# Kernel tuning notes

Measured on AMD Instinct MI355X. Metric: run time of the kernel, lower is better.

Reference implementation:

```python
import jax, jax.numpy as jnp
import numpy as np

H = 1024
NUM_HEADS = 16
HEAD_DIM = H // NUM_HEADS
EPS = 1e-6
GEN_E, GEN_IE = 8, 4096 // 8     # general experts, per-expert intermediate
MOD_E, MOD_IE = 4, 4096 // 4     # per-modality experts, per-expert intermediate


def layernorm(x, g, b):
    m = jnp.mean(x, axis=-1, keepdims=True)
    v = jnp.mean((x - m) ** 2, axis=-1, keepdims=True)
    return (x - m) * jax.lax.rsqrt(v + EPS) * g + b


def attention(x, qkv_w, qkv_b, proj_w, proj_b):
    B, N, _ = x.shape
    qkv = (x @ qkv_w + qkv_b).reshape(B, N, 3, NUM_HEADS, HEAD_DIM)
    qkv = jnp.transpose(qkv, (2, 0, 3, 1, 4))  # [3,B,h,N,d]
    q, k, v = qkv[0], qkv[1], qkv[2]
    scale = HEAD_DIM ** -0.5
    attn = jax.nn.softmax(jnp.einsum('bhnd,bhmd->bhnm', q, k) * scale, axis=-1)
    out = jnp.einsum('bhnm,bhmd->bhnd', attn, v)
    out = jnp.transpose(out, (0, 2, 1, 3)).reshape(B, N, H)
    return out @ proj_w + proj_b


def routed_mlp(x, position_ids, gate_up, down, ie):
    # expert_id = position % num_experts; compute all experts then select per token
    # (avoids materializing per-token [T,H,2I] gathered weights).
    E = gate_up.shape[0]
    eids = position_ids % E  # [B,N]
    gu = jnp.einsum('bnh,ehi->bnei', x, gate_up)              # [B,N,E,2*ie]
    gu = jnp.take_along_axis(gu, eids[..., None, None], axis=2)[:, :, 0]
    gate, up = gu[..., :ie], gu[..., ie:]
    inter = jax.nn.silu(gate) * up                             # [B,N,ie]
    dn = jnp.einsum('bni,eih->bneh', inter, down)              # [B,N,E,H]
    return jnp.take_along_axis(dn, eids[..., None, None], axis=2)[:, :, 0]


def setup_inputs() -> dict:
    key = jax.random.key(0)
    ks = jax.random.split(key, 16)
    B, N = 2, 2048
    inp = {
        'x': jax.random.normal(ks[0], (B, N, H), jnp.float32),
        'qkv_w': jax.random.normal(ks[1], (H, 3 * H), jnp.float32) * 0.02,
        'qkv_b': jnp.zeros((3 * H,), jnp.float32),
        'proj_w': jax.random.normal(ks[2], (H, H), jnp.float32) * 0.02,
        'proj_b': jnp.zeros((H,), jnp.float32),
        'ln1_g': jnp.ones((H,), jnp.float32), 'ln1_b': jnp.zeros((H,), jnp.float32),
        'ln2_g': jnp.ones((H,), jnp.float32), 'ln2_b': jnp.zeros((H,), jnp.float32),
        'ln3_g': jnp.ones((H,), jnp.float32), 'ln3_b': jnp.zeros((H,), jnp.float32),
        'gen_gu': jax.random.normal(ks[3], (GEN_E, H, 2 * GEN_IE), jnp.float32) * 0.02,
        'gen_dn': jax.random.normal(ks[4], (GEN_E, GEN_IE, H), jnp.float32) * 0.02,
        'text_gu': jax.random.normal(ks[5], (MOD_E, H, 2 * MOD_IE), jnp.float32) * 0.02,
        'text_dn': jax.random.normal(ks[6], (MOD_E, MOD_IE, H), jnp.float32) * 0.02,
        'img_gu': jax.random.normal(ks[7], (MOD_E, H, 2 * MOD_IE), jnp.float32) * 0.02,
        'img_dn': jax.random.normal(ks[8], (MOD_E, MOD_IE, H), jnp.float32) * 0.02,
        'aud_gu': jax.random.normal(ks[9], (MOD_E, H, 2 * MOD_IE), jnp.float32) * 0.02,
        'aud_dn': jax.random.normal(ks[10], (MOD_E, MOD_IE, H), jnp.float32) * 0.02,
        'vid_gu': jax.random.normal(ks[11], (MOD_E, H, 2 * MOD_IE), jnp.float32) * 0.02,
        'vid_dn': jax.random.normal(ks[12], (MOD_E, MOD_IE, H), jnp.float32) * 0.02,
        'modality_ids': jax.random.randint(ks[13], (B, N), 0, 4, jnp.int32),
        'position_ids': jnp.arange(B * N, dtype=jnp.int32).reshape(B, N),
    }
    return inp


def reference(x, qkv_w, qkv_b, proj_w, proj_b,
              ln1_g, ln1_b, ln2_g, ln2_b, ln3_g, ln3_b,
              gen_gu, gen_dn, text_gu, text_dn, img_gu, img_dn,
              aud_gu, aud_dn, vid_gu, vid_dn,
              modality_ids, position_ids):
    x = x + attention(layernorm(x, ln1_g, ln1_b), qkv_w, qkv_b, proj_w, proj_b)
    x = x + routed_mlp(layernorm(x, ln2_g, ln2_b), position_ids, gen_gu, gen_dn, GEN_IE)
    normed = layernorm(x, ln3_g, ln3_b)
    tm = (modality_ids == 0)[..., None].astype(x.dtype)
    im = (modality_ids == 1)[..., None].astype(x.dtype)
    am = (modality_ids == 2)[..., None].astype(x.dtype)
    vm = (modality_ids == 3)[..., None].astype(x.dtype)
    x = x + (routed_mlp(normed, position_ids, text_gu, text_dn, MOD_IE) * tm
             + routed_mlp(normed, position_ids, img_gu, img_dn, MOD_IE) * im
             + routed_mlp(normed, position_ids, aud_gu, aud_dn, MOD_IE) * am
             + routed_mlp(normed, position_ids, vid_gu, vid_dn, MOD_IE) * vm)
    return x
```

## Files before the change

kernel.cpp:

```cpp
#include <hip/hip_runtime.h>

#define T_TOKENS 4096
#define HDIM 1024

typedef __attribute__((ext_vector_type(8))) short bf16x8;
typedef __attribute__((ext_vector_type(4))) float f32x4;

#define EXP2F(x) __builtin_amdgcn_exp2f(x)

static __device__ inline unsigned short f2bf(float f) {
  unsigned u = __float_as_uint(f);
  unsigned r = (u + 0x7FFFu + ((u >> 16) & 1u)) >> 16;
  return (unsigned short)r;
}
static __device__ __forceinline__ unsigned cvtpk(float lo, float hi) {
  unsigned r;
  asm("v_cvt_pk_bf16_f32 %0, %1, %2" : "=v"(r) : "v"(lo), "v"(hi));
  return r;
}
static __device__ __forceinline__ void gl16(const void* g, void* l) {
  __builtin_amdgcn_global_load_lds((const __attribute__((address_space(1))) void*)g,
                                   (__attribute__((address_space(3))) void*)l, 16, 0, 0);
}

__launch_bounds__(256)
__global__ void ln_kernel(const float* __restrict__ in, const float* __restrict__ g,
                          const float* __restrict__ b, unsigned short* __restrict__ out) {
  const int row = blockIdx.x;
  const int tid = threadIdx.x;
  const long base = (long)row * HDIM;
  float4 v = *(const float4*)(in + base + tid * 4);
  __shared__ float red[256];
  red[tid] = v.x + v.y + v.z + v.w;
  __syncthreads();
  for (int st = 128; st > 0; st >>= 1) {
    if (tid < st) red[tid] += red[tid + st];
    __syncthreads();
  }
  const float mean = red[0] * (1.f / HDIM);
  __syncthreads();
  const float dx = v.x - mean, dy = v.y - mean, dz = v.z - mean, dw = v.w - mean;
  red[tid] = dx * dx + dy * dy + dz * dz + dw * dw;
  __syncthreads();
  for (int st = 128; st > 0; st >>= 1) {
    if (tid < st) red[tid] += red[tid + st];
    __syncthreads();
  }
  const float rstd = rsqrtf(red[0] * (1.f / HDIM) + 1e-6f);
  const int c = tid * 4;
  const float4 g4 = *(const float4*)(g + c);
  const float4 b4 = *(const float4*)(b + c);
  uint2 o;
  o.x = cvtpk(dx * rstd * g4.x + b4.x, dy * rstd * g4.y + b4.y);
  o.y = cvtpk(dz * rstd * g4.z + b4.z, dw * rstd * g4.w + b4.w);
  *(uint2*)(out + base + c) = o;
}

__launch_bounds__(256)
__global__ void build_groups(const int* __restrict__ pids, const int* __restrict__ mids,
                             int* __restrict__ gen_cnt, int* __restrict__ gen_list,
                             int* __restrict__ mod_cnt, int* __restrict__ mod_list) {
  const int t = blockIdx.x * 256 + threadIdx.x;
  if (t >= T_TOKENS) return;
  const int p = pids[t];
  const int ge = p & 7;
  int s = atomicAdd(&gen_cnt[ge], 1);
  if (s < 512) gen_list[ge * 512 + s] = t;
  const int g = mids[t] * 4 + (p & 3);
  s = atomicAdd(&mod_cnt[g], 1);
  if (s < 1024) mod_list[g * 1024 + s] = t;
}

__launch_bounds__(256)
__global__ void convert_w(const float* __restrict__ W, unsigned short* __restrict__ Wt,
                          int K, int N) {
  const long zo = (long)blockIdx.z * K * N;
  const float* Wp = W + zo;
  unsigned short* Wo = Wt + zo;
  const int n0 = blockIdx.x * 64, k0 = blockIdx.y * 64;
  __shared__ float T[64][65];
  const int tid = threadIdx.x;
#pragma unroll
  for (int i = 0; i < 4; ++i) {
    const int item = tid + i * 256;
    const int kk = item >> 4, c4 = (item & 15) * 4;
    const float4 v = *(const float4*)(Wp + (long)(k0 + kk) * N + n0 + c4);
    T[c4 + 0][kk] = v.x; T[c4 + 1][kk] = v.y; T[c4 + 2][kk] = v.z; T[c4 + 3][kk] = v.w;
  }
  __syncthreads();
#pragma unroll
  for (int i = 0; i < 4; ++i) {
    const int item = tid + i * 256;
    const int nn = item >> 4, k4 = (item & 15) * 4;
    uint2 p;
    p.x = cvtpk(T[nn][k4 + 0], T[nn][k4 + 1]);
    p.y = cvtpk(T[nn][k4 + 2], T[nn][k4 + 3]);
    *(uint2*)(Wo + (long)(n0 + nn) * K + k0 + k4) = p;
  }
}

enum { MODE_DENSE = 0, MODE_GEN = 1, MODE_MOD = 2 };
enum { OM_F32R = 0, OM_BF16 = 1, OM_QKV = 2 };

template <int MODE, int OMODE, bool WBF16, bool BIAS>
__launch_bounds__(256)
__global__ void mgemm(const unsigned short* __restrict__ A,
                      const void* __restrict__ w0, const float* __restrict__ w1,
                      const float* __restrict__ w2, const float* __restrict__ w3,
                      long wstep, const float* __restrict__ bias,
                      const float* __restrict__ resid, void* __restrict__ Cout,
                      unsigned short* __restrict__ qb, unsigned short* __restrict__ kb,
                      unsigned short* __restrict__ vtb,
                      int K, int N,
                      const int* __restrict__ cnts, const int* __restrict__ rowlist,
                      int cap) {
  const int z = blockIdx.z;
  const int n0 = blockIdx.x * 128;
  const int m0 = blockIdx.y * 128;

  int Meff = 1 << 30;
  const int* list = nullptr;
  if constexpr (MODE != MODE_DENSE) {
    Meff = cnts[z];
    if (m0 >= Meff) return;
    list = rowlist + z * cap;
  }

  constexpr int BUFSZ = 128 * 64 * 2;
  __shared__ char As[2 * BUFSZ];
  __shared__ char Bs[2 * BUFSZ];

  const int tid = threadIdx.x;
  const int w = tid >> 6;
  const int lane = tid & 63;
  const int wm = w >> 1, wn = w & 1;
  const int srow = lane >> 3, sc = lane & 7;

  const unsigned short* asrc[4];
#pragma unroll
  for (int i = 0; i < 4; ++i) {
    const int r = w * 32 + i * 8 + srow;
    long tok;
    if constexpr (MODE == MODE_DENSE) {
      tok = m0 + r;
    } else {
      int gm = m0 + r;
      if (gm >= Meff) gm = Meff - 1;
      tok = (long)list[gm];
    }
    asrc[i] = A + tok * (long)K + (sc ^ (r & 7)) * 8;
  }

  const unsigned short* bsrc[4];
  const float* bptr[4];
  int boff[4];
  if constexpr (WBF16) {
    const unsigned short* W = (const unsigned short*)w0;
    if constexpr (MODE != MODE_DENSE) W += (long)z * wstep;
#pragma unroll
    for (int i = 0; i < 4; ++i) {
      const int r = w * 32 + i * 8 + srow;
      bsrc[i] = W + (long)(n0 + r) * K + (sc ^ (r & 7)) * 8;
    }
  } else {
    const float* W;
    if constexpr (MODE == MODE_MOD) {
      const int mm = z >> 2;
      const float* basep = (mm == 0) ? (const float*)w0 : (mm == 1) ? w1 : (mm == 2) ? w2 : w3;
      W = basep + (long)(z & 3) * wstep;
    } else {
      W = (const float*)w0 + (MODE != MODE_DENSE ? (long)z * wstep : 0);
    }
#pragma unroll
    for (int j = 0; j < 4; ++j) {
      const int item = tid + j * 256;
      const int kc = item >> 7;
      const int nl = item & 127;
      bptr[j] = W + (long)(kc * 8) * N + n0 + nl;
      boff[j] = (nl * 128 + kc * 16) ^ ((nl & 7) << 4);
    }
  }

  f32x4 acc[4][4] = {};
  float kv[4][8];

  auto stageA = [&](int s, int kt) {
#pragma unroll
    for (int i = 0; i < 4; ++i) gl16(asrc[i] + kt, As + s * BUFSZ + w * 4096 + i * 1024);
  };
  auto stageB16 = [&](int s, int kt) {
#pragma unroll
    for (int i = 0; i < 4; ++i) gl16(bsrc[i] + kt, Bs + s * BUFSZ + w * 4096 + i * 1024);
  };
  auto loadB = [&](int kt) {
#pragma unroll
    for (int j = 0; j < 4; ++j) {
      const float* bp = bptr[j] + (long)kt * N;
#pragma unroll
      for (int u = 0; u < 8; ++u) kv[j][u] = bp[(long)u * N];
    }
  };
  auto writeB = [&](int s) {
#pragma unroll
    for (int j = 0; j < 4; ++j) {
      uint4 p;
      p.x = cvtpk(kv[j][0], kv[j][1]);
      p.y = cvtpk(kv[j][2], kv[j][3]);
      p.z = cvtpk(kv[j][4], kv[j][5]);
      p.w = cvtpk(kv[j][6], kv[j][7]);
      *(uint4*)(Bs + s * BUFSZ + boff[j]) = p;
    }
  };
  auto compute = [&](int s) {
#pragma unroll
    for (int kk = 0; kk < 2; ++kk) {
      const int kb2 = kk * 64 + (lane >> 4) * 16;
      bf16x8 af[4], bfr[4];
#pragma unroll
      for (int f = 0; f < 4; ++f) {
        const int ar = wm * 64 + f * 16 + (lane & 15);
        af[f] = *(bf16x8*)(As + s * BUFSZ + ((ar * 128 + kb2) ^ ((ar & 7) << 4)));
        const int br = wn * 64 + f * 16 + (lane & 15);
        bfr[f] = *(bf16x8*)(Bs + s * BUFSZ + ((br * 128 + kb2) ^ ((br & 7) << 4)));
      }
#pragma unroll
      for (int mf = 0; mf < 4; ++mf)
#pragma unroll
        for (int nf = 0; nf < 4; ++nf)
          acc[mf][nf] =
              __builtin_amdgcn_mfma_f32_16x16x32_bf16(af[mf], bfr[nf], acc[mf][nf], 0, 0, 0);
    }
  };

  const int nk = K >> 6;
  stageA(0, 0);
  if constexpr (WBF16) {
    stageB16(0, 0);
  } else {
    loadB(0);
    writeB(0);
  }
  __syncthreads();

  int sel = 0;
  for (int t = 0; t < nk; ++t) {
    const bool more = (t + 1) < nk;
    const int ktn = (t + 1) * 64;
    if (more) {
      stageA(sel ^ 1, ktn);
      if constexpr (WBF16) stageB16(sel ^ 1, ktn);
      else loadB(ktn);
    }
    compute(sel);
    if constexpr (!WBF16) {
      if (more) writeB(sel ^ 1);
    }
    __syncthreads();
    sel ^= 1;
  }

  const int lr4 = (lane >> 4) * 4;
  const int lc = lane & 15;
#pragma unroll
  for (int mf = 0; mf < 4; ++mf) {
#pragma unroll
    for (int r = 0; r < 4; ++r) {
      const int gm = m0 + wm * 64 + mf * 16 + lr4 + r;
      long orow;
      if constexpr (MODE == MODE_DENSE) {
        orow = gm;
      } else {
        if (gm >= Meff) continue;
        orow = (long)list[gm];
      }
#pragma unroll
      for (int nf = 0; nf < 4; ++nf) {
        const int gc = n0 + wn * 64 + nf * 16 + lc;
        float val = acc[mf][nf][r];
        if constexpr (BIAS) val += bias[gc];
        if constexpr (OMODE == OM_F32R) {
          val += resid[orow * (long)N + gc];
          ((float*)Cout)[orow * (long)N + gc] = val;
        } else if constexpr (OMODE == OM_BF16) {
          ((unsigned short*)Cout)[orow * (long)N + gc] = f2bf(val);
        } else {
          const int bb = (int)(orow >> 11), tl = (int)orow & 2047;
          const int seg = gc >> 10, hc = gc & 1023, h = hc >> 6, d = hc & 63;
          if (seg == 0)
            qb[(((long)(bb * 16 + h) * 2048) + tl) * 64 + d] = f2bf(val * 0.18033688011112042f);
          else if (seg == 1)
            kb[(((long)(bb * 16 + h) * 2048) + tl) * 64 + d] = f2bf(val);
          else
            vtb[((long)(bb * 16 + h) * 64 + d) * 2048 + tl] = f2bf(val);
        }
      }
    }
  }
}

__launch_bounds__(256)
__global__ void attn_kernel(const unsigned short* __restrict__ Qb,
                            const unsigned short* __restrict__ Kb,
                            const unsigned short* __restrict__ Vtb,
                            unsigned short* __restrict__ out) {
  const int qt = blockIdx.x;
  const int bh = blockIdx.y;
  const int b = bh >> 4, h = bh & 15;
  const int tid = threadIdx.x;
  const int w = tid >> 6;
  const int lane = tid & 63;
  const int g = lane >> 4;
  const int q = lane & 15;

  __shared__ char Ksb[128 * 128];
  __shared__ char Vsb[64 * 256];
  __shared__ char Psb[4 * 16 * 256];
  char* Pwb = Psb + w * 4096;

  const unsigned short* Qh = Qb + ((long)(b * 16 + h) * 2048 + qt * 64) * 64;
  const unsigned short* Kh = Kb + (long)(b * 16 + h) * 2048 * 64;
  const unsigned short* Vh = Vtb + (long)(b * 16 + h) * 64 * 2048;

  bf16x8 qf[2];
#pragma unroll
  for (int kst = 0; kst < 2; ++kst)
    qf[kst] = *(const bf16x8*)(Qh + (w * 16 + q) * 64 + kst * 32 + g * 8);

  const unsigned short* ksrc[4];
  const unsigned short* vsrc[4];
  char* kld = Ksb + w * 4096;
  char* vld = Vsb + w * 4096;
#pragma unroll
  for (int i = 0; i < 4; ++i) {
    const int r = w * 32 + i * 8 + (lane >> 3);
    ksrc[i] = Kh + (long)r * 64 + ((lane & 7) ^ (r & 7)) * 8;
    const int d = w * 16 + i * 4 + (lane >> 4);
    vsrc[i] = Vh + (long)d * 2048 + ((lane & 15) ^ (d & 7)) * 8;
  }

  float m_run = -1e30f, l_run = 0.f;
  f32x4 acc[4] = {};
  const int qsw = (q & 7) << 4;

  for (int kt = 0; kt < 16; ++kt) {
    __syncthreads();
#pragma unroll
    for (int i = 0; i < 4; ++i) gl16(ksrc[i] + (long)kt * 128 * 64, kld + i * 1024);
#pragma unroll
    for (int i = 0; i < 4; ++i) gl16(vsrc[i] + kt * 128, vld + i * 1024);
    __syncthreads();

    f32x4 sf[8];
#pragma unroll
    for (int f = 0; f < 8; ++f) {
      const int krow = f * 16 + q;
      const int sw = (krow & 7) << 4;
      const bf16x8 k0 = *(bf16x8*)(Ksb + krow * 128 + ((g * 16) ^ sw));
      const bf16x8 k1 = *(bf16x8*)(Ksb + krow * 128 + ((64 + g * 16) ^ sw));
      f32x4 t = {};
      t = __builtin_amdgcn_mfma_f32_16x16x32_bf16(k0, qf[0], t, 0, 0, 0);
      sf[f] = __builtin_amdgcn_mfma_f32_16x16x32_bf16(k1, qf[1], t, 0, 0, 0);
    }

    float mx = sf[0][0];
#pragma unroll
    for (int f = 0; f < 8; ++f) {
      mx = fmaxf(mx, fmaxf(fmaxf(sf[f][0], sf[f][1]), fmaxf(sf[f][2], sf[f][3])));
    }
    mx = fmaxf(mx, __shfl_xor(mx, 16));
    mx = fmaxf(mx, __shfl_xor(mx, 32));
    const float mn = fmaxf(m_run, mx);
    const float alpha = EXP2F(m_run - mn);
    m_run = mn;

    float ls = 0.f;
#pragma unroll
    for (int f = 0; f < 8; ++f) {
#pragma unroll
      for (int r = 0; r < 4; ++r) {
        sf[f][r] = EXP2F(sf[f][r] - mn);
      }
      ls += (sf[f][0] + sf[f][1]) + (sf[f][2] + sf[f][3]);
    }
    ls += __shfl_xor(ls, 16);
    ls += __shfl_xor(ls, 32);
    l_run = l_run * alpha + ls;

#pragma unroll
    for (int f = 0; f < 8; ++f) {
      const unsigned p0 = cvtpk(sf[f][0], sf[f][1]);
      const unsigned p1 = cvtpk(sf[f][2], sf[f][3]);
      const int base = f * 32 + g * 8;
      *(unsigned*)(Pwb + q * 256 + ((base) ^ qsw)) = p0;
      *(unsigned*)(Pwb + q * 256 + ((base + 4) ^ qsw)) = p1;
    }

#pragma unroll
    for (int r = 0; r < 4; ++r) {
      const float aO = __shfl(alpha, g * 4 + r, 64);
      acc[0][r] *= aO; acc[1][r] *= aO; acc[2][r] *= aO; acc[3][r] *= aO;
    }

#pragma unroll
    for (int kst = 0; kst < 4; ++kst) {
      const bf16x8 pa = *(bf16x8*)(Pwb + q * 256 + ((kst * 64 + g * 16) ^ qsw));
#pragma unroll
      for (int df = 0; df < 4; ++df) {
        const int vrow = df * 16 + q;
        const int vsw = (vrow & 7) << 4;
        const bf16x8 vf = *(bf16x8*)(Vsb + vrow * 256 + ((kst * 64 + g * 16) ^ vsw));
        acc[df] = __builtin_amdgcn_mfma_f32_16x16x32_bf16(pa, vf, acc[df], 0, 0, 0);
      }
    }
  }

  float linv[4];
#pragma unroll
  for (int r = 0; r < 4; ++r) linv[r] = 1.f / __shfl(l_run, g * 4 + r, 64);
  unsigned short* op = out + (long)(b * 2048 + qt * 64 + w * 16) * 1024 + h * 64;
#pragma unroll
  for (int df = 0; df < 4; ++df)
#pragma unroll
    for (int r = 0; r < 4; ++r) {
      const int row = g * 4 + r;
      op[(long)row * 1024 + df * 16 + q] = f2bf(acc[df][r] * linv[r]);
    }
}

__launch_bounds__(256)
__global__ void silu_bf(const unsigned short* __restrict__ gu, unsigned short* __restrict__ inter,
                        int IE2, int IE, int shift) {
  const int total = T_TOKENS << shift;
  for (int idx = blockIdx.x * 256 + threadIdx.x; idx < total; idx += gridDim.x * 256) {
    const int t = idx >> shift;
    const int r8 = (idx & ((1 << shift) - 1)) * 8;
    const unsigned short* gp = gu + (long)t * IE2 + r8;
    const uint4 gg = *(const uint4*)gp;
    const uint4 uu = *(const uint4*)(gp + IE);
    const unsigned gw[4] = {gg.x, gg.y, gg.z, gg.w};
    const unsigned uw[4] = {uu.x, uu.y, uu.z, uu.w};
    uint4 o;
    unsigned ow[4];
#pragma unroll
    for (int qq = 0; qq < 4; ++qq) {
      const float g0 = __uint_as_float(gw[qq] << 16);
      const float g1 = __uint_as_float(gw[qq] & 0xffff0000u);
      const float u0 = __uint_as_float(uw[qq] << 16);
      const float u1 = __uint_as_float(uw[qq] & 0xffff0000u);
      const float r0 = g0 / (1.f + __expf(-g0)) * u0;
      const float r1 = g1 / (1.f + __expf(-g1)) * u1;
      ow[qq] = cvtpk(r0, r1);
    }
    o.x = ow[0]; o.y = ow[1]; o.z = ow[2]; o.w = ow[3];
    *(uint4*)(inter + (long)t * IE + r8) = o;
  }
}

extern "C" void kernel_launch(void* const* d_in, const int* in_sizes, int n_in,
                              void* d_out, int out_size, void* d_ws, size_t ws_size,
                              hipStream_t stream) {
  const float* x       = (const float*)d_in[0];
  const float* qkv_w   = (const float*)d_in[1];
  const float* qkv_b   = (const float*)d_in[2];
  const float* proj_w  = (const float*)d_in[3];
  const float* proj_b  = (const float*)d_in[4];
  const float* ln1_g   = (const float*)d_in[5];
  const float* ln1_b   = (const float*)d_in[6];
  const float* ln2_g   = (const float*)d_in[7];
  const float* ln2_b   = (const float*)d_in[8];
  const float* ln3_g   = (const float*)d_in[9];
  const float* ln3_b   = (const float*)d_in[10];
  const float* gen_gu  = (const float*)d_in[11];
  const float* gen_dn  = (const float*)d_in[12];
  const float* text_gu = (const float*)d_in[13];
  const float* text_dn = (const float*)d_in[14];
  const float* img_gu  = (const float*)d_in[15];
  const float* img_dn  = (const float*)d_in[16];
  const float* aud_gu  = (const float*)d_in[17];
  const float* aud_dn  = (const float*)d_in[18];
  const float* vid_gu  = (const float*)d_in[19];
  const float* vid_dn  = (const float*)d_in[20];
  const int* mids      = (const int*)d_in[21];
  const int* pids      = (const int*)d_in[22];
  float* out = (float*)d_out;
  char* ws = (char*)d_ws;

  const unsigned long MB = 1ul << 20;
  unsigned short* lnb   = (unsigned short*)(ws);
  unsigned short* Qb    = (unsigned short*)(ws + 8 * MB);
  unsigned short* Kb    = (unsigned short*)(ws + 16 * MB);
  unsigned short* Vtb   = (unsigned short*)(ws + 24 * MB);
  unsigned short* attno = (unsigned short*)(ws + 32 * MB);
  unsigned short* wqkv  = (unsigned short*)(ws + 40 * MB);
  unsigned short* wproj = (unsigned short*)(ws + 46 * MB);
  unsigned short* wggu  = (unsigned short*)(ws + 48 * MB);
  unsigned short* wgdn  = (unsigned short*)(ws + 64 * MB);
  int* gen_cnt  = (int*)(ws + 72 * MB);
  int* mod_cnt  = gen_cnt + 8;
  int* gen_list = gen_cnt + 32;
  int* mod_list = gen_list + 8 * 512;
  unsigned short* guo    = Qb;
  unsigned short* intero = Vtb;

  (void)hipMemsetAsync(gen_cnt, 0, (8 + 16) * sizeof(int), stream);
  build_groups<<<16, 256, 0, stream>>>(pids, mids, gen_cnt, gen_list, mod_cnt, mod_list);

  convert_w<<<dim3(48, 16, 1), 256, 0, stream>>>(qkv_w, wqkv, 1024, 3072);
  convert_w<<<dim3(16, 16, 1), 256, 0, stream>>>(proj_w, wproj, 1024, 1024);
  convert_w<<<dim3(16, 16, 8), 256, 0, stream>>>(gen_gu, wggu, 1024, 1024);
  convert_w<<<dim3(16, 8, 8), 256, 0, stream>>>(gen_dn, wgdn, 512, 1024);

  ln_kernel<<<4096, 256, 0, stream>>>(x, ln1_g, ln1_b, lnb);
  mgemm<MODE_DENSE, OM_QKV, true, true><<<dim3(24, 32, 1), 256, 0, stream>>>(
      lnb, wqkv, nullptr, nullptr, nullptr, 0L, qkv_b, nullptr, nullptr,
      Qb, Kb, Vtb, 1024, 3072, nullptr, nullptr, 0);
  attn_kernel<<<dim3(32, 32, 1), 256, 0, stream>>>(Qb, Kb, Vtb, attno);
  mgemm<MODE_DENSE, OM_F32R, true, true><<<dim3(8, 32, 1), 256, 0, stream>>>(
      attno, wproj, nullptr, nullptr, nullptr, 0L, proj_b, x, out,
      nullptr, nullptr, nullptr, 1024, 1024, nullptr, nullptr, 0);

  ln_kernel<<<4096, 256, 0, stream>>>(out, ln2_g, ln2_b, lnb);
  mgemm<MODE_GEN, OM_BF16, true, false><<<dim3(8, 4, 8), 256, 0, stream>>>(
      lnb, wggu, nullptr, nullptr, nullptr, (long)1024 * 1024, nullptr, nullptr, guo,
      nullptr, nullptr, nullptr, 1024, 1024, gen_cnt, gen_list, 512);
  silu_bf<<<1024, 256, 0, stream>>>(guo, intero, 1024, 512, 6);
  mgemm<MODE_GEN, OM_F32R, true, false><<<dim3(8, 4, 8), 256, 0, stream>>>(
      intero, wgdn, nullptr, nullptr, nullptr, (long)1024 * 512, nullptr, out, out,
      nullptr, nullptr, nullptr, 512, 1024, gen_cnt, gen_list, 512);

  ln_kernel<<<4096, 256, 0, stream>>>(out, ln3_g, ln3_b, lnb);
  mgemm<MODE_MOD, OM_BF16, false, false><<<dim3(16, 8, 16), 256, 0, stream>>>(
      lnb, text_gu, img_gu, aud_gu, vid_gu, (long)1024 * 2048, nullptr, nullptr, guo,
      nullptr, nullptr, nullptr, 1024, 2048, mod_cnt, mod_list, 1024);
  silu_bf<<<2048, 256, 0, stream>>>(guo, intero, 2048, 1024, 7);
  mgemm<MODE_MOD, OM_F32R, false, false><<<dim3(8, 8, 16), 256, 0, stream>>>(
      intero, text_dn, img_dn, aud_dn, vid_dn, (long)1024 * 1024, nullptr, out, out,
      nullptr, nullptr, nullptr, 1024, 1024, mod_cnt, mod_list, 1024);
}
```

Baseline: 385.0 us.

## Double-buffer K/V tiles in attention, lazy rescale, XCD-aware block remap

Restructures the attention kernel to use 64-key tiles held in two LDS buffers. The next tile is prefetched while the current one is computed, replacing the two barriers per iteration with one. It skips the running-max rescale of the accumulator unless the new max exceeds the old by more than 8 (log2 units). It also pads the P buffer stride instead of XOR swizzling, and remaps block indices so heads group per XCD for L2 locality. In exchange the loop runs twice as many iterations with smaller MFMA batches, and the lazy rescale relies on exp2 headroom in fp32.

```diff
diff --git a/kernel.cpp b/kernel.cpp
--- a/kernel.cpp
+++ b/kernel.cpp
@@ -303,8 +303,10 @@
                             const unsigned short* __restrict__ Kb,
                             const unsigned short* __restrict__ Vtb,
                             unsigned short* __restrict__ out) {
-  const int qt = blockIdx.x;
-  const int bh = blockIdx.y;
+  const int lin = blockIdx.x + blockIdx.y * 32;
+  const int xcd = lin & 7, rank = lin >> 3;
+  const int bh = xcd * 4 + (rank >> 5);
+  const int qt = rank & 31;
   const int b = bh >> 4, h = bh & 15;
   const int tid = threadIdx.x;
   const int w = tid >> 6;
@@ -312,10 +314,13 @@
   const int g = lane >> 4;
   const int q = lane & 15;
 
-  __shared__ char Ksb[128 * 128];
-  __shared__ char Vsb[64 * 256];
-  __shared__ char Psb[4 * 16 * 256];
-  char* Pwb = Psb + w * 4096;
+  constexpr int KBUF = 64 * 128;
+  constexpr int VBUF = 64 * 128;
+  constexpr int PSTR = 144;
+  __shared__ char Ksb[2 * KBUF];
+  __shared__ char Vsb[2 * VBUF];
+  __shared__ char Psb[4 * 16 * PSTR];
+  char* Pwb = Psb + w * 16 * PSTR;
 
   const unsigned short* Qh = Qb + ((long)(b * 16 + h) * 2048 + qt * 64) * 64;
   const unsigned short* Kh = Kb + (long)(b * 16 + h) * 2048 * 64;
@@ -326,92 +331,93 @@
   for (int kst = 0; kst < 2; ++kst)
     qf[kst] = *(const bf16x8*)(Qh + (w * 16 + q) * 64 + kst * 32 + g * 8);
 
-  const unsigned short* ksrc[4];
-  const unsigned short* vsrc[4];
-  char* kld = Ksb + w * 4096;
-  char* vld = Vsb + w * 4096;
-#pragma unroll
-  for (int i = 0; i < 4; ++i) {
-    const int r = w * 32 + i * 8 + (lane >> 3);
+  const unsigned short* ksrc[2];
+  const unsigned short* vsrc[2];
+#pragma unroll
+  for (int i = 0; i < 2; ++i) {
+    const int r = w * 16 + i * 8 + (lane >> 3);
     ksrc[i] = Kh + (long)r * 64 + ((lane & 7) ^ (r & 7)) * 8;
-    const int d = w * 16 + i * 4 + (lane >> 4);
-    vsrc[i] = Vh + (long)d * 2048 + ((lane & 15) ^ (d & 7)) * 8;
-  }
+    const int d = w * 16 + i * 8 + (lane >> 3);
+    vsrc[i] = Vh + (long)d * 2048 + ((lane & 7) ^ (d & 7)) * 8;
+  }
+  auto stage = [&](int s, int t) {
+#pragma unroll
+    for (int i = 0; i < 2; ++i) {
+      gl16(ksrc[i] + (long)t * 64 * 64, Ksb + s * KBUF + w * 2048 + i * 1024);
+      gl16(vsrc[i] + t * 64, Vsb + s * VBUF + w * 2048 + i * 1024);
+    }
+  };
 
   float m_run = -1e30f, l_run = 0.f;
   f32x4 acc[4] = {};
-  const int qsw = (q & 7) << 4;
-
-  for (int kt = 0; kt < 16; ++kt) {
-    __syncthreads();
-#pragma unroll
-    for (int i = 0; i < 4; ++i) gl16(ksrc[i] + (long)kt * 128 * 64, kld + i * 1024);
-#pragma unroll
-    for (int i = 0; i < 4; ++i) gl16(vsrc[i] + kt * 128, vld + i * 1024);
-    __syncthreads();
-
-    f32x4 sf[8];
-#pragma unroll
-    for (int f = 0; f < 8; ++f) {
+
+  stage(0, 0);
+  __syncthreads();
+
+  for (int kt = 0; kt < 32; ++kt) {
+    const int cur = kt & 1;
+    if (kt + 1 < 32) stage(cur ^ 1, kt + 1);
+
+    f32x4 sf[4];
+#pragma unroll
+    for (int f = 0; f < 4; ++f) {
       const int krow = f * 16 + q;
       const int sw = (krow & 7) << 4;
-      const bf16x8 k0 = *(bf16x8*)(Ksb + krow * 128 + ((g * 16) ^ sw));
-      const bf16x8 k1 = *(bf16x8*)(Ksb + krow * 128 + ((64 + g * 16) ^ sw));
+      const bf16x8 k0 = *(bf16x8*)(Ksb + cur * KBUF + krow * 128 + ((g * 16) ^ sw));
+      const bf16x8 k1 = *(bf16x8*)(Ksb + cur * KBUF + krow * 128 + ((64 + g * 16) ^ sw));
       f32x4 t = {};
       t = __builtin_amdgcn_mfma_f32_16x16x32_bf16(k0, qf[0], t, 0, 0, 0);
       sf[f] = __builtin_amdgcn_mfma_f32_16x16x32_bf16(k1, qf[1], t, 0, 0, 0);
     }
 
-    float mx = sf[0][0];
-#pragma unroll
-    for (int f = 0; f < 8; ++f) {
-      mx = fmaxf(mx, fmaxf(fmaxf(sf[f][0], sf[f][1]), fmaxf(sf[f][2], sf[f][3])));
-    }
-    mx = fmaxf(mx, __shfl_xor(mx, 16));
-    mx = fmaxf(mx, __shfl_xor(mx, 32));
-    const float mn = fmaxf(m_run, mx);
-    const float alpha = EXP2F(m_run - mn);
-    m_run = mn;
+    float pm = sf[0][0];
+#pragma unroll
+    for (int f = 0; f < 4; ++f)
+      pm = fmaxf(pm, fmaxf(fmaxf(sf[f][0], sf[f][1]), fmaxf(sf[f][2], sf[f][3])));
+    pm = fmaxf(pm, __shfl_xor(pm, 16));
+    pm = fmaxf(pm, __shfl_xor(pm, 32));
+    float al = 1.f;
+    if (!__all(pm - m_run <= 8.f)) {
+      const float mn = fmaxf(m_run, pm);
+      al = EXP2F(m_run - mn);
+      m_run = mn;
+#pragma unroll
+      for (int r = 0; r < 4; ++r) {
+        const float aO = __shfl(al, g * 4 + r, 64);
+        acc[0][r] *= aO; acc[1][r] *= aO; acc[2][r] *= aO; acc[3][r] *= aO;
+      }
+    }
 
     float ls = 0.f;
 #pragma unroll
-    for (int f = 0; f < 8; ++f) {
-#pragma unroll
-      for (int r = 0; r < 4; ++r) {
-        sf[f][r] = EXP2F(sf[f][r] - mn);
-      }
+    for (int f = 0; f < 4; ++f) {
+#pragma unroll
+      for (int r = 0; r < 4; ++r) sf[f][r] = EXP2F(sf[f][r] - m_run);
       ls += (sf[f][0] + sf[f][1]) + (sf[f][2] + sf[f][3]);
     }
     ls += __shfl_xor(ls, 16);
     ls += __shfl_xor(ls, 32);
-    l_run = l_run * alpha + ls;
-
-#pragma unroll
-    for (int f = 0; f < 8; ++f) {
-      const unsigned p0 = cvtpk(sf[f][0], sf[f][1]);
-      const unsigned p1 = cvtpk(sf[f][2], sf[f][3]);
-      const int base = f * 32 + g * 8;
-      *(unsigned*)(Pwb + q * 256 + ((base) ^ qsw)) = p0;
-      *(unsigned*)(Pwb + q * 256 + ((base + 4) ^ qsw)) = p1;
-    }
-
-#pragma unroll
-    for (int r = 0; r < 4; ++r) {
-      const float aO = __shfl(alpha, g * 4 + r, 64);
-      acc[0][r] *= aO; acc[1][r] *= aO; acc[2][r] *= aO; acc[3][r] *= aO;
-    }
-
-#pragma unroll
-    for (int kst = 0; kst < 4; ++kst) {
-      const bf16x8 pa = *(bf16x8*)(Pwb + q * 256 + ((kst * 64 + g * 16) ^ qsw));
+    l_run = l_run * al + ls;
+
+#pragma unroll
+    for (int f = 0; f < 4; ++f) {
+      const int base = q * PSTR + f * 32 + g * 8;
+      *(unsigned*)(Pwb + base) = cvtpk(sf[f][0], sf[f][1]);
+      *(unsigned*)(Pwb + base + 4) = cvtpk(sf[f][2], sf[f][3]);
+    }
+
+#pragma unroll
+    for (int kst = 0; kst < 2; ++kst) {
+      const bf16x8 pa = *(bf16x8*)(Pwb + q * PSTR + kst * 64 + g * 16);
 #pragma unroll
       for (int df = 0; df < 4; ++df) {
         const int vrow = df * 16 + q;
         const int vsw = (vrow & 7) << 4;
-        const bf16x8 vf = *(bf16x8*)(Vsb + vrow * 256 + ((kst * 64 + g * 16) ^ vsw));
+        const bf16x8 vf = *(bf16x8*)(Vsb + cur * VBUF + vrow * 128 + ((kst * 64 + g * 16) ^ vsw));
         acc[df] = __builtin_amdgcn_mfma_f32_16x16x32_bf16(pa, vf, acc[df], 0, 0, 0);
       }
     }
+    __syncthreads();
   }
 
   float linv[4];
```

After: 393.9 us. 2.3% more time.

## Remap attention blocks per XCD, lazily rescale softmax, pad P LDS buffer

Applied to the files above, without the earlier changes.

Remaps the attention grid so that blocks landing on the same XCD (round-robin by linear block id) share the same batch-head, which should improve L2 reuse of K/V. Adds a conditional online-softmax rescale that only updates the running max and rescales the accumulators when the new max exceeds the old one by more than a threshold, skipping exp and multiply work in the common case. Replaces the XOR-swizzled P staging buffer with a padded row stride. The lazy rescale lets exponentials grow up to 2^8 before renormalisation, so precision relies on that bound. The padded layout may change LDS bank-conflict behaviour.

```diff
diff --git a/kernel.cpp b/kernel.cpp
--- a/kernel.cpp
+++ b/kernel.cpp
@@ -303,8 +303,10 @@
                             const unsigned short* __restrict__ Kb,
                             const unsigned short* __restrict__ Vtb,
                             unsigned short* __restrict__ out) {
-  const int qt = blockIdx.x;
-  const int bh = blockIdx.y;
+  const int lin = blockIdx.x + blockIdx.y * 32;
+  const int xcd = lin & 7, rank = lin >> 3;
+  const int bh = xcd * 4 + (rank >> 5);
+  const int qt = rank & 31;
   const int b = bh >> 4, h = bh & 15;
   const int tid = threadIdx.x;
   const int w = tid >> 6;
@@ -312,10 +314,11 @@
   const int g = lane >> 4;
   const int q = lane & 15;
 
+  constexpr int PSTR = 272;
   __shared__ char Ksb[128 * 128];
   __shared__ char Vsb[64 * 256];
-  __shared__ char Psb[4 * 16 * 256];
-  char* Pwb = Psb + w * 4096;
+  __shared__ char Psb[4 * 16 * PSTR];
+  char* Pwb = Psb + w * 16 * PSTR;
 
   const unsigned short* Qh = Qb + ((long)(b * 16 + h) * 2048 + qt * 64) * 64;
   const unsigned short* Kh = Kb + (long)(b * 16 + h) * 2048 * 64;
@@ -340,7 +343,6 @@
 
   float m_run = -1e30f, l_run = 0.f;
   f32x4 acc[4] = {};
-  const int qsw = (q & 7) << 4;
 
   for (int kt = 0; kt < 16; ++kt) {
     __syncthreads();
@@ -362,48 +364,45 @@
       sf[f] = __builtin_amdgcn_mfma_f32_16x16x32_bf16(k1, qf[1], t, 0, 0, 0);
     }
 
-    float mx = sf[0][0];
+    float pm = fmaxf(fmaxf(sf[0][0], sf[0][1]), fmaxf(sf[0][2], sf[0][3]));
+#pragma unroll
+    for (int f = 1; f < 8; ++f)
+      pm = fmaxf(pm, fmaxf(fmaxf(sf[f][0], sf[f][1]), fmaxf(sf[f][2], sf[f][3])));
+    pm = fmaxf(pm, __shfl_xor(pm, 16));
+    pm = fmaxf(pm, __shfl_xor(pm, 32));
+    float al = 1.f;
+    if (!__all(pm - m_run <= 8.f)) {
+      const float mn = fmaxf(m_run, pm);
+      al = EXP2F(m_run - mn);
+      m_run = mn;
+#pragma unroll
+      for (int r = 0; r < 4; ++r) {
+        const float aO = __shfl(al, g * 4 + r, 64);
+        acc[0][r] *= aO; acc[1][r] *= aO; acc[2][r] *= aO; acc[3][r] *= aO;
+      }
+    }
+
+    float ls = 0.f;
 #pragma unroll
     for (int f = 0; f < 8; ++f) {
-      mx = fmaxf(mx, fmaxf(fmaxf(sf[f][0], sf[f][1]), fmaxf(sf[f][2], sf[f][3])));
-    }
-    mx = fmaxf(mx, __shfl_xor(mx, 16));
-    mx = fmaxf(mx, __shfl_xor(mx, 32));
-    const float mn = fmaxf(m_run, mx);
-    const float alpha = EXP2F(m_run - mn);
-    m_run = mn;
-
-    float ls = 0.f;
-#pragma unroll
-    for (int f = 0; f < 8; ++f) {
-#pragma unroll
-      for (int r = 0; r < 4; ++r) {
-        sf[f][r] = EXP2F(sf[f][r] - mn);
-      }
+#pragma unroll
+      for (int r = 0; r < 4; ++r) sf[f][r] = EXP2F(sf[f][r] - m_run);
       ls += (sf[f][0] + sf[f][1]) + (sf[f][2] + sf[f][3]);
     }
     ls += __shfl_xor(ls, 16);
     ls += __shfl_xor(ls, 32);
-    l_run = l_run * alpha + ls;
+    l_run = l_run * al + ls;
 
 #pragma unroll
     for (int f = 0; f < 8; ++f) {
-      const unsigned p0 = cvtpk(sf[f][0], sf[f][1]);
-      const unsigned p1 = cvtpk(sf[f][2], sf[f][3]);
-      const int base = f * 32 + g * 8;
-      *(unsigned*)(Pwb + q * 256 + ((base) ^ qsw)) = p0;
-      *(unsigned*)(Pwb + q * 256 + ((base + 4) ^ qsw)) = p1;
-    }
-
-#pragma unroll
-    for (int r = 0; r < 4; ++r) {
-      const float aO = __shfl(alpha, g * 4 + r, 64);
-      acc[0][r] *= aO; acc[1][r] *= aO; acc[2][r] *= aO; acc[3][r] *= aO;
+      const int base = q * PSTR + f * 32 + g * 8;
+      *(unsigned*)(Pwb + base) = cvtpk(sf[f][0], sf[f][1]);
+      *(unsigned*)(Pwb + base + 4) = cvtpk(sf[f][2], sf[f][3]);
     }
 
 #pragma unroll
     for (int kst = 0; kst < 4; ++kst) {
-      const bf16x8 pa = *(bf16x8*)(Pwb + q * 256 + ((kst * 64 + g * 16) ^ qsw));
+      const bf16x8 pa = *(bf16x8*)(Pwb + q * PSTR + kst * 64 + g * 16);
 #pragma unroll
       for (int df = 0; df < 4; ++df) {
         const int vrow = df * 16 + q;
```

Result: no change. 378.4 us (median of 3 runs) (-1.7%).
